# Kernel optimization log

Measured on AMD Instinct MI355X. Metric: run time of the kernel, lower is better.

## Reference

```python
import jax, jax.numpy as jnp
from jax import lax
import numpy as np

DIM = 768
NUM_HEADS = 12
HEAD_DIM = DIM // NUM_HEADS
POOL = 8
LAM1_INIT = 0.5
LAM2_INIT = 0.5
EPS = 1e-6


def rmsnorm(x, w):
    # x / (||x||_2 / sqrt(d) + eps) * w
    d = x.shape[-1]
    rms = jnp.sqrt(jnp.sum(x * x, axis=-1, keepdims=True)) / jnp.sqrt(jnp.asarray(d, x.dtype))
    return x / (rms + EPS) * w


def setup_inputs() -> dict:
    key = jax.random.key(0)
    ks = jax.random.split(key, 10)
    B, H, W = 32, 32, 32
    N = H * W
    x = jax.random.normal(ks[0], (B, N, DIM), dtype=jnp.float32)
    Wqkv = jax.random.normal(ks[1], (3 * DIM, DIM), dtype=jnp.float32) * 0.02
    Wproj = jax.random.normal(ks[2], (DIM, DIM), dtype=jnp.float32) * 0.02
    bproj = jnp.zeros((DIM,), dtype=jnp.float32)
    Wpos = jax.random.normal(ks[3], (HEAD_DIM, HEAD_DIM), dtype=jnp.float32) * 0.02
    Wneg = jax.random.normal(ks[4], (HEAD_DIM, HEAD_DIM), dtype=jnp.float32) * 0.02
    conv_w = jax.random.normal(ks[5], (HEAD_DIM, 1, 3, 3), dtype=jnp.float32) * 0.1  # depthwise OIHW
    lam1 = jnp.asarray(LAM1_INIT, dtype=jnp.float32)
    lam2 = jnp.asarray(LAM2_INIT, dtype=jnp.float32)
    norm1_w = jnp.ones((HEAD_DIM,), dtype=jnp.float32)
    norm2_w = jnp.ones((HEAD_DIM,), dtype=jnp.float32)
    return {"x": x, "Wqkv": Wqkv, "Wproj": Wproj, "bproj": bproj, "Wpos": Wpos,
            "Wneg": Wneg, "conv_w": conv_w, "lam1": lam1, "lam2": lam2,
            "norm1_w": norm1_w, "norm2_w": norm2_w, "H": H, "W": W}


def reference(x, Wqkv, Wproj, bproj, Wpos, Wneg, conv_w, lam1, lam2, norm1_w, norm2_w, H, W):
    B, N, C = x.shape
    h, hd, p = NUM_HEADS, HEAD_DIM, POOL
    scale = hd ** -0.5
    # qkv projection -> [3, B, h, N, hd]
    qkv = (x @ Wqkv.T).reshape(B, N, 3, h, hd).transpose(2, 0, 3, 1, 4)
    q, k, v = qkv[0], qkv[1], qkv[2]
    # depthwise conv + GELU on q in spatial form
    q2 = q.reshape(B, h, H, W, hd).transpose(0, 1, 4, 2, 3).reshape(B * h, hd, H, W)
    qe = lax.conv_general_dilated(q2, conv_w, window_strides=(1, 1), padding='SAME',
                                  feature_group_count=hd,
                                  dimension_numbers=('NCHW', 'OIHW', 'NCHW'))
    qe = jax.nn.gelu(qe, approximate=False)
    # adaptive avg pool to (p, p): exact since H % p == 0
    qp = qe.reshape(B * h, hd, p, H // p, p, W // p).mean(axis=(3, 5))
    t_base = qp.reshape(B, h, hd, p, p).transpose(0, 1, 3, 4, 2).reshape(B, h, p * p, hd)
    # dynamic e+/e- embeddings from global query
    gq = q.mean(axis=2)  # [B, h, hd]
    t_pos = t_base + (gq @ Wpos.T)[:, :, None, :]
    t_neg = t_base + (gq @ Wneg.T)[:, :, None, :]
    # stage 1: pooled contrast tokens attend to k/v
    attn_pos = jax.nn.softmax(jnp.einsum('bhmd,bhnd->bhmn', t_pos, k) * scale, axis=-1)
    v_hat_pos = attn_pos @ v  # [B, h, p*p, hd]
    attn_neg = jax.nn.softmax(jnp.einsum('bhmd,bhnd->bhmn', t_neg, k) * scale, axis=-1)
    v_hat_neg = attn_neg @ v
    v_contrast = rmsnorm(v_hat_pos - lam1 * v_hat_neg, norm1_w) * (1.0 - LAM1_INIT)
    # stage 2: q attends to contrast tokens
    attn1 = jax.nn.softmax(jnp.einsum('bhnd,bhmd->bhnm', q, t_pos) * scale, axis=-1)
    attn2 = jax.nn.softmax(jnp.einsum('bhnd,bhmd->bhnm', q, t_neg) * scale, axis=-1)
    out_patch = (attn1 - lam2 * attn2) @ v_contrast  # [B, h, N, hd]
    out_patch = rmsnorm(out_patch, norm2_w) * (1.0 - LAM2_INIT)
    out_patch = out_patch.transpose(0, 2, 1, 3).reshape(B, N, C)
    out = out_patch @ Wproj.T + bproj
    return out
```

## Files before the change

kernel.cpp:

```cpp
#include <hip/hip_runtime.h>
#include <hip/hip_bf16.h>


typedef __attribute__((ext_vector_type(8))) short short8;
typedef __attribute__((ext_vector_type(4))) short bf16x4;
typedef __attribute__((ext_vector_type(4))) float f32x4;

#define DEV static __device__ __forceinline__

DEV unsigned short f2bf(float f) {
  unsigned int b; __builtin_memcpy(&b, &f, 4);
  unsigned int r = (b + 0x7FFFu + ((b >> 16) & 1u)) >> 16;
  return (unsigned short)r;
}
DEV float bf2f(unsigned short u) {
  unsigned int b = ((unsigned int)u) << 16;
  float f; __builtin_memcpy(&f, &b, 4);
  return f;
}

DEV void gload16(const unsigned short* g, unsigned short* l) {
  __builtin_amdgcn_global_load_lds(
      (const __attribute__((address_space(1))) unsigned int*)g,
      (__attribute__((address_space(3))) unsigned int*)l, 16, 0, 0);
}

DEV void bar() {
  asm volatile("" ::: "memory");
  __builtin_amdgcn_s_barrier();
  asm volatile("" ::: "memory");
}
DEV void wait_vm4() { asm volatile("s_waitcnt vmcnt(4)" ::: "memory"); __builtin_amdgcn_sched_barrier(0); }
DEV void wait_vm0() { asm volatile("s_waitcnt vmcnt(0)" ::: "memory"); __builtin_amdgcn_sched_barrier(0); }
DEV void wait_lgkm0() { asm volatile("s_waitcnt lgkmcnt(0)" ::: "memory"); __builtin_amdgcn_sched_barrier(0); }

constexpr size_t SZ_QKV = (size_t)32 * 12 * 1024 * 64 * 2;
constexpr size_t OFF_Q   = 0;
constexpr size_t OFF_K   = OFF_Q + SZ_QKV;
constexpr size_t OFF_VT  = OFF_K + SZ_QKV;
constexpr size_t OFF_TPB = OFF_VT + SZ_QKV;
constexpr size_t OFF_TNB = OFF_TPB + 3145728;
constexpr size_t OFF_VCT = OFF_TNB + 3145728;
constexpr size_t OFF_OP  = OFF_VCT + 6291456;
constexpr size_t OFF_XB  = OFF_OP + SZ_QKV;
constexpr size_t OFF_WQ  = OFF_XB + SZ_QKV;
constexpr size_t OFF_WP  = OFF_WQ + 3538944;
constexpr size_t OFF_EP  = OFF_WP + 1179648;
constexpr size_t OFF_EN  = OFF_EP + 98304;

__global__ __launch_bounds__(256) void cast_kernel(const float* __restrict__ src,
                                                   unsigned short* __restrict__ dst, int n4) {
  int i = blockIdx.x * 256 + threadIdx.x;
  if (i >= n4) return;
  float4 v = reinterpret_cast<const float4*>(src)[i];
  ushort4 o;
  o.x = f2bf(v.x); o.y = f2bf(v.y); o.z = f2bf(v.z); o.w = f2bf(v.w);
  reinterpret_cast<ushort4*>(dst)[i] = o;
}

DEV void stage_ht(const unsigned short* __restrict__ G, unsigned short* shbase,
                  int grow0, int k0, int htrow0, int w, int lane) {
  const int rl = lane >> 3;
  const int ck = (lane & 7) ^ rl;
  const unsigned short* s0 = G + (size_t)(grow0 + htrow0 + w * 16 + rl) * 768 + k0 + ck * 8;
  gload16(s0, shbase + (htrow0 + w * 16) * 64);
  gload16(s0 + (size_t)8 * 768, shbase + (htrow0 + w * 16 + 8) * 64);
}

__global__ __launch_bounds__(512, 2) void gemm_qkv_kernel(const unsigned short* __restrict__ A,
    const unsigned short* __restrict__ Bm, unsigned short* __restrict__ q,
    unsigned short* __restrict__ k, unsigned short* __restrict__ vt) {
  __shared__ __align__(16) unsigned short sh[65536];
  const int t = threadIdx.x;
  const int lane = t & 63;
  const int w = t >> 6;
  const int wm = w >> 2, wn = w & 3;
  const int l = lane & 15, g = lane >> 4;
  const int id = blockIdx.x;
  const int swz = (id & 7) * 144 + (id >> 3);
  const int rt = swz / 9, ct = swz % 9;
  const int row0 = rt * 256, col0 = ct * 256;

  f32x4 acc[8][4];
#pragma unroll
  for (int i = 0; i < 8; ++i)
#pragma unroll
    for (int j = 0; j < 4; ++j) acc[i][j] = (f32x4){0.f, 0.f, 0.f, 0.f};

  stage_ht(A, sh, row0, 0, 0, w, lane);
  stage_ht(A, sh, row0, 0, 128, w, lane);
  stage_ht(Bm, sh + 32768, col0, 0, 0, w, lane);
  stage_ht(Bm, sh + 32768, col0, 0, 128, w, lane);
  stage_ht(Bm, sh + 32768 + 16384, col0, 64, 0, w, lane);
  stage_ht(Bm, sh + 32768 + 16384, col0, 64, 128, w, lane);
  wait_vm4();
  bar();

  for (int m = 0; m < 12; ++m) {
    const int d = m & 1;
    const unsigned short* Ab = sh + d * 16384;
    const unsigned short* Bb = sh + 32768 + d * 16384;
    short8 af[4][2], bf0[2][2], bf1[2][2];
#pragma unroll
    for (int mt = 0; mt < 4; ++mt)
#pragma unroll
      for (int kc = 0; kc < 2; ++kc) {
        const int r = wm * 128 + mt * 16 + l;
        af[mt][kc] = *reinterpret_cast<const short8*>(Ab + r * 64 + (((kc << 2) | g) ^ (r & 7)) * 8);
      }
#pragma unroll
    for (int nt = 0; nt < 2; ++nt)
#pragma unroll
      for (int kc = 0; kc < 2; ++kc) {
        const int r = wn * 64 + nt * 16 + l;
        bf0[nt][kc] = *reinterpret_cast<const short8*>(Bb + r * 64 + (((kc << 2) | g) ^ (r & 7)) * 8);
      }
    if (m + 1 < 12) stage_ht(A, sh + (d ^ 1) * 16384, row0, (m + 1) * 64, 0, w, lane);
    bar();
    __builtin_amdgcn_s_setprio(1);
#pragma unroll
    for (int kc = 0; kc < 2; ++kc)
#pragma unroll
      for (int mt = 0; mt < 4; ++mt)
#pragma unroll
        for (int nt = 0; nt < 2; ++nt)
          acc[mt][nt] = __builtin_amdgcn_mfma_f32_16x16x32_bf16(af[mt][kc], bf0[nt][kc], acc[mt][nt], 0, 0, 0);
    __builtin_amdgcn_s_setprio(0);
    bar();
#pragma unroll
    for (int nt = 0; nt < 2; ++nt)
#pragma unroll
      for (int kc = 0; kc < 2; ++kc) {
        const int r = wn * 64 + 32 + nt * 16 + l;
        bf1[nt][kc] = *reinterpret_cast<const short8*>(Bb + r * 64 + (((kc << 2) | g) ^ (r & 7)) * 8);
      }
    if (m + 1 < 12) stage_ht(A, sh + (d ^ 1) * 16384, row0, (m + 1) * 64, 128, w, lane);
    bar();
    __builtin_amdgcn_s_setprio(1);
#pragma unroll
    for (int kc = 0; kc < 2; ++kc)
#pragma unroll
      for (int mt = 0; mt < 4; ++mt)
#pragma unroll
        for (int nt = 0; nt < 2; ++nt)
          acc[mt][2 + nt] = __builtin_amdgcn_mfma_f32_16x16x32_bf16(af[mt][kc], bf1[nt][kc], acc[mt][2 + nt], 0, 0, 0);
    __builtin_amdgcn_s_setprio(0);
    bar();
#pragma unroll
    for (int mt = 0; mt < 4; ++mt)
#pragma unroll
      for (int kc = 0; kc < 2; ++kc) {
        const int r = wm * 128 + 64 + mt * 16 + l;
        af[mt][kc] = *reinterpret_cast<const short8*>(Ab + r * 64 + (((kc << 2) | g) ^ (r & 7)) * 8);
      }
    if (m + 2 < 12) stage_ht(Bm, sh + 32768 + d * 16384, col0, (m + 2) * 64, 0, w, lane);
    bar();
    __builtin_amdgcn_s_setprio(1);
#pragma unroll
    for (int kc = 0; kc < 2; ++kc)
#pragma unroll
      for (int mt = 0; mt < 4; ++mt)
#pragma unroll
        for (int nt = 0; nt < 2; ++nt)
          acc[4 + mt][2 + nt] = __builtin_amdgcn_mfma_f32_16x16x32_bf16(af[mt][kc], bf1[nt][kc], acc[4 + mt][2 + nt], 0, 0, 0);
    __builtin_amdgcn_s_setprio(0);
    bar();
    if (m + 2 < 12) stage_ht(Bm, sh + 32768 + d * 16384, col0, (m + 2) * 64, 128, w, lane);
    bar();
    __builtin_amdgcn_s_setprio(1);
#pragma unroll
    for (int kc = 0; kc < 2; ++kc)
#pragma unroll
      for (int mt = 0; mt < 4; ++mt)
#pragma unroll
        for (int nt = 0; nt < 2; ++nt)
          acc[4 + mt][nt] = __builtin_amdgcn_mfma_f32_16x16x32_bf16(af[mt][kc], bf0[nt][kc], acc[4 + mt][nt], 0, 0, 0);
    __builtin_amdgcn_s_setprio(0);
    if (m < 11) {
      if (m == 10) wait_vm0(); else wait_vm4();
    }
    bar();
  }

  const int s_ = ct / 3;
  if (s_ == 2) {
#pragma unroll
    for (int ni = 0; ni < 4; ++ni) {
      const int colg = (ct % 3) * 256 + wn * 64 + ni * 16 + l;
      const int head = colg >> 6, dd = colg & 63;
#pragma unroll
      for (int mi = 0; mi < 8; ++mi) {
        const int row = row0 + wm * 128 + mi * 16 + (g << 2);
        const int b = row >> 10, n = row & 1023;
        ushort4 pk;
        pk.x = f2bf(acc[mi][ni][0]); pk.y = f2bf(acc[mi][ni][1]);
        pk.z = f2bf(acc[mi][ni][2]); pk.w = f2bf(acc[mi][ni][3]);
        *reinterpret_cast<ushort4*>(vt + ((((size_t)b * 12 + head) * 64 + dd) << 10) + n) = pk;
      }
    }
  } else {
    unsigned short* dst = (s_ == 0) ? q : k;
#pragma unroll
    for (int ni = 0; ni < 4; ++ni) {
      const int colg = (ct % 3) * 256 + wn * 64 + ni * 16 + l;
      const int head = colg >> 6, dd = colg & 63;
#pragma unroll
      for (int mi = 0; mi < 8; ++mi) {
#pragma unroll
        for (int r = 0; r < 4; ++r) {
          const int row = row0 + wm * 128 + mi * 16 + (g << 2) + r;
          const int b = row >> 10, n = row & 1023;
          dst[(((size_t)b * 12 + head) * 1024 + n) * 64 + dd] = f2bf(acc[mi][ni][r]);
        }
      }
    }
  }
}

__global__ __launch_bounds__(256) void gq_embed_kernel(const unsigned short* __restrict__ qg,
    const float* __restrict__ Wpos, const float* __restrict__ Wneg,
    float* __restrict__ ep, float* __restrict__ en) {
  const int bh = blockIdx.x;
  const unsigned short* qp = qg + (size_t)bh * 65536;
  __shared__ float red2[32][64];
  __shared__ float gq_s[64];
  const int t = threadIdx.x;
  const int c8 = (t & 7) << 3;
  const int part = t >> 3;
  float s[8] = {0.f, 0.f, 0.f, 0.f, 0.f, 0.f, 0.f, 0.f};
  for (int i = 0; i < 32; ++i) {
    const short8 v = *reinterpret_cast<const short8*>(qp + (size_t)(part * 32 + i) * 64 + c8);
#pragma unroll
    for (int j = 0; j < 8; ++j) s[j] += bf2f((unsigned short)v[j]);
  }
#pragma unroll
  for (int j = 0; j < 8; ++j) red2[part][c8 + j] = s[j];
  __syncthreads();
  if (t < 64) {
    float s2 = 0.f;
    for (int p = 0; p < 32; ++p) s2 += red2[p][t];
    gq_s[t] = s2 * (1.0f / 1024.0f);
  }
  __syncthreads();
  if (t < 128) {
    const int d2 = t & 63;
    const float* Wm = (t < 64) ? Wpos : Wneg;
    float e = 0.f;
    for (int dd = 0; dd < 64; ++dd) e += gq_s[dd] * Wm[d2 * 64 + dd];
    (t < 64 ? ep : en)[bh * 64 + d2] = e;
  }
}

__global__ __launch_bounds__(256) void conv_pool_kernel(const unsigned short* __restrict__ qg,
    const float* __restrict__ conv_w, const float* __restrict__ ep,
    const float* __restrict__ en, unsigned short* __restrict__ t_pos,
    unsigned short* __restrict__ t_neg) {
  const int bh = blockIdx.x;
  const int quad = blockIdx.y;
  const unsigned short* qp = qg + (size_t)bh * 65536;
  __shared__ float pool_s[16][64];
  const int t = threadIdx.x;
  const int dg = t & 7, sp = t >> 3;
  const int d0 = dg << 3;
  float cw[3][3][8];
#pragma unroll
  for (int ky = 0; ky < 3; ++ky)
#pragma unroll
    for (int kx = 0; kx < 3; ++kx)
#pragma unroll
      for (int j = 0; j < 8; ++j)
        cw[ky][kx][j] = conv_w[(d0 + j) * 9 + ky * 3 + kx];
#pragma unroll
  for (int pyl = 0; pyl < 2; ++pyl) {
    float win[8] = {0.f, 0.f, 0.f, 0.f, 0.f, 0.f, 0.f, 0.f};
#pragma unroll
    for (int iy = 0; iy < 4; ++iy) {
      const int y = quad * 8 + pyl * 4 + iy;
      float a[8] = {0.f, 0.f, 0.f, 0.f, 0.f, 0.f, 0.f, 0.f};
#pragma unroll
      for (int ky = 0; ky < 3; ++ky) {
        const int yy = y + ky - 1;
        if (yy < 0 || yy > 31) continue;
#pragma unroll
        for (int kx = 0; kx < 3; ++kx) {
          const int xx = sp + kx - 1;
          if (xx < 0 || xx > 31) continue;
          const short8 v = *reinterpret_cast<const short8*>(qp + (size_t)(yy * 32 + xx) * 64 + d0);
#pragma unroll
          for (int j = 0; j < 8; ++j) a[j] += bf2f((unsigned short)v[j]) * cw[ky][kx][j];
        }
      }
#pragma unroll
      for (int j = 0; j < 8; ++j)
        win[j] += 0.5f * a[j] * (1.0f + erff(a[j] * 0.70710678118654752440f));
    }
#pragma unroll
    for (int j = 0; j < 8; ++j) {
      win[j] += __shfl_xor(win[j], 8);
      win[j] += __shfl_xor(win[j], 16);
    }
    if ((sp & 3) == 0) {
      const int px = sp >> 2;
#pragma unroll
      for (int j = 0; j < 8; ++j) pool_s[pyl * 8 + px][d0 + j] = win[j];
    }
  }
  __syncthreads();
#pragma unroll
  for (int i = 0; i < 4; ++i) {
    const int idx = i * 256 + t;
    const int m = idx >> 6, dd = idx & 63;
    const int mg = quad * 16 + m;
    const float base = pool_s[m][dd] * (1.0f / 16.0f);
    t_pos[(size_t)bh * 4096 + mg * 64 + dd] = f2bf(base + ep[bh * 64 + dd]);
    t_neg[(size_t)bh * 4096 + mg * 64 + dd] = f2bf(base + en[bh * 64 + dd]);
  }
}

__global__ __launch_bounds__(256) void stage1_kernel(const unsigned short* __restrict__ kg,
    const unsigned short* __restrict__ vtg, const unsigned short* __restrict__ tpb,
    const unsigned short* __restrict__ tnb, const float* __restrict__ lam1p,
    const float* __restrict__ norm1_w, unsigned short* __restrict__ vct) {
  const int bh = blockIdx.x;
  __shared__ unsigned short tp[64 * 72], tn[64 * 72];
  __shared__ __align__(16) unsigned short Ks[2][4096];
  __shared__ __align__(16) unsigned short Vts[2][4096];
  const int t = threadIdx.x;
  const int lane = t & 63;
  const int w = t >> 6;
  const int l = lane & 15, g = lane >> 4;
  const size_t kbase = (size_t)bh * 65536;
  const int rl = lane >> 3, ck = (lane & 7) ^ rl;

  for (int L = t; L < 512; L += 256) {
    const int r = L >> 3, c = (L & 7) << 3;
    *reinterpret_cast<short8*>(tp + r * 72 + c) =
        *reinterpret_cast<const short8*>(tpb + (size_t)bh * 4096 + r * 64 + c);
    *reinterpret_cast<short8*>(tn + r * 72 + c) =
        *reinterpret_cast<const short8*>(tnb + (size_t)bh * 4096 + r * 64 + c);
  }
  auto stageKV = [&](int buf, int n0) {
    const unsigned short* ksrc = kg + kbase + (size_t)(n0 + w * 16 + rl) * 64 + ck * 8;
    gload16(ksrc, &Ks[buf][(w * 16) * 64]);
    gload16(ksrc + (size_t)8 * 64, &Ks[buf][(w * 16 + 8) * 64]);
    const unsigned short* vsrc = vtg + kbase + (size_t)(w * 16 + rl) * 1024 + n0 + ck * 8;
    gload16(vsrc, &Vts[buf][(w * 16) * 64]);
    gload16(vsrc + (size_t)8 * 1024, &Vts[buf][(w * 16 + 8) * 64]);
  };
  stageKV(0, 0);
  __syncthreads();

  short8 tf[2][2];
#pragma unroll
  for (int h = 0; h < 2; ++h) {
    tf[0][h] = *reinterpret_cast<const short8*>(tp + (w * 16 + l) * 72 + h * 32 + g * 8);
    tf[1][h] = *reinterpret_cast<const short8*>(tn + (w * 16 + l) * 72 + h * 32 + g * 8);
  }
  float Mo[2] = {-1e30f, -1e30f}, Lo[2] = {0.f, 0.f};
  f32x4 acc[2][4];
#pragma unroll
  for (int pp = 0; pp < 2; ++pp)
#pragma unroll
    for (int dt = 0; dt < 4; ++dt) acc[pp][dt] = (f32x4){0.f, 0.f, 0.f, 0.f};

  for (int it = 0; it < 16; ++it) {
    const int buf = it & 1;
    if (it < 15) stageKV(buf ^ 1, (it + 1) * 64);
    short8 kf[4][2];
#pragma unroll
    for (int tile = 0; tile < 4; ++tile)
#pragma unroll
      for (int h = 0; h < 2; ++h) {
        const int R = tile * 16 + l;
        kf[tile][h] = *reinterpret_cast<const short8*>(&Ks[buf][R * 64 + ((((h << 2) | g)) ^ (l & 7)) * 8]);
      }
    bf16x4 pf[2][4];
#pragma unroll
    for (int pp = 0; pp < 2; ++pp) {
      f32x4 s[4];
#pragma unroll
      for (int tile = 0; tile < 4; ++tile) {
        s[tile] = (f32x4){0.f, 0.f, 0.f, 0.f};
#pragma unroll
        for (int h = 0; h < 2; ++h)
          s[tile] = __builtin_amdgcn_mfma_f32_16x16x32_bf16(kf[tile][h], tf[pp][h], s[tile], 0, 0, 0);
      }
      float p[4][4];
      float tmax = -1e30f;
#pragma unroll
      for (int tile = 0; tile < 4; ++tile)
#pragma unroll
        for (int r = 0; r < 4; ++r) {
          const float v = s[tile][r] * 0.125f;
          p[tile][r] = v;
          tmax = fmaxf(tmax, v);
        }
      tmax = fmaxf(tmax, __shfl_xor(tmax, 16));
      tmax = fmaxf(tmax, __shfl_xor(tmax, 32));
      const float nm = fmaxf(Mo[pp], tmax);
      const float al = __expf(Mo[pp] - nm);
      Mo[pp] = nm;
      float ps = 0.f;
#pragma unroll
      for (int tile = 0; tile < 4; ++tile)
#pragma unroll
        for (int r = 0; r < 4; ++r) {
          const float e = __expf(p[tile][r] - nm);
          p[tile][r] = e;
          ps += e;
        }
      ps += __shfl_xor(ps, 16);
      ps += __shfl_xor(ps, 32);
      Lo[pp] = Lo[pp] * al + ps;
#pragma unroll
      for (int tile = 0; tile < 4; ++tile) {
        bf16x4 pk;
        pk[0] = (short)f2bf(p[tile][0]); pk[1] = (short)f2bf(p[tile][1]);
        pk[2] = (short)f2bf(p[tile][2]); pk[3] = (short)f2bf(p[tile][3]);
        pf[pp][tile] = pk;
      }
      float ar[4];
#pragma unroll
      for (int r = 0; r < 4; ++r) ar[r] = __shfl(al, 4 * g + r);
#pragma unroll
      for (int dt = 0; dt < 4; ++dt)
#pragma unroll
        for (int r = 0; r < 4; ++r) acc[pp][dt][r] *= ar[r];
    }
#pragma unroll
    for (int tile = 0; tile < 4; ++tile)
#pragma unroll
      for (int dt = 0; dt < 4; ++dt) {
        const int R = dt * 16 + l;
        const bf16x4 vf = *reinterpret_cast<const bf16x4*>(
            &Vts[buf][R * 64 + (((2 * tile + (g >> 1)) ^ (l & 7)) * 8) + (g & 1) * 4]);
        acc[0][dt] = __builtin_amdgcn_mfma_f32_16x16x16bf16_1k(pf[0][tile], vf, acc[0][dt], 0, 0, 0);
        acc[1][dt] = __builtin_amdgcn_mfma_f32_16x16x16bf16_1k(pf[1][tile], vf, acc[1][dt], 0, 0, 0);
      }
    __syncthreads();
  }
  const float inv0 = 1.f / Lo[0], inv1 = 1.f / Lo[1];
  float i1r[4], i2r[4];
#pragma unroll
  for (int r = 0; r < 4; ++r) {
    i1r[r] = __shfl(inv0, 4 * g + r);
    i2r[r] = __shfl(inv1, 4 * g + r);
  }
  const float lam1 = lam1p[0];
  float od[4][4], ss[4] = {0.f, 0.f, 0.f, 0.f};
#pragma unroll
  for (int dt = 0; dt < 4; ++dt)
#pragma unroll
    for (int r = 0; r < 4; ++r) {
      const float v = acc[0][dt][r] * i1r[r] - lam1 * (acc[1][dt][r] * i2r[r]);
      od[dt][r] = v;
      ss[r] += v * v;
    }
#pragma unroll
  for (int r = 0; r < 4; ++r) {
    ss[r] += __shfl_xor(ss[r], 1);
    ss[r] += __shfl_xor(ss[r], 2);
    ss[r] += __shfl_xor(ss[r], 4);
    ss[r] += __shfl_xor(ss[r], 8);
  }
  float sc[4];
#pragma unroll
  for (int r = 0; r < 4; ++r) sc[r] = 0.5f / (sqrtf(ss[r]) * 0.125f + 1e-6f);
  const int mb = w * 16 + 4 * g;
#pragma unroll
  for (int dt = 0; dt < 4; ++dt) {
    const int dd = dt * 16 + l;
    const float nw = norm1_w[dd];
    ushort4 pk;
    pk.x = f2bf(od[dt][0] * sc[0] * nw);
    pk.y = f2bf(od[dt][1] * sc[1] * nw);
    pk.z = f2bf(od[dt][2] * sc[2] * nw);
    pk.w = f2bf(od[dt][3] * sc[3] * nw);
    *reinterpret_cast<ushort4*>(vct + (size_t)bh * 4096 + dd * 64 + mb) = pk;
  }
}

__global__ __launch_bounds__(256) void stage2_kernel(const unsigned short* __restrict__ qg,
    const unsigned short* __restrict__ tpb, const unsigned short* __restrict__ tnb,
    const unsigned short* __restrict__ vctg, const float* __restrict__ lam2p,
    const float* __restrict__ norm2_w, unsigned short* __restrict__ opb) {
  const int bh = blockIdx.x;
  const int q0 = blockIdx.y * 64;
  __shared__ unsigned short tp[64 * 72], tn[64 * 72], Qs[64 * 72], Vc[64 * 72];
  const int t = threadIdx.x;
  const int lane = t & 63;
  const int w = t >> 6;
  const int l = lane & 15, g = lane >> 4;
  for (int L = t; L < 512; L += 256) {
    const int r = L >> 3, c = (L & 7) << 3;
    *reinterpret_cast<short8*>(tp + r * 72 + c) =
        *reinterpret_cast<const short8*>(tpb + (size_t)bh * 4096 + r * 64 + c);
    *reinterpret_cast<short8*>(tn + r * 72 + c) =
        *reinterpret_cast<const short8*>(tnb + (size_t)bh * 4096 + r * 64 + c);
    *reinterpret_cast<short8*>(Qs + r * 72 + c) =
        *reinterpret_cast<const short8*>(qg + (size_t)bh * 65536 + (size_t)(q0 + r) * 64 + c);
    *reinterpret_cast<short8*>(Vc + r * 72 + c) =
        *reinterpret_cast<const short8*>(vctg + (size_t)bh * 4096 + r * 64 + c);
  }
  __syncthreads();
  short8 qf[2];
#pragma unroll
  for (int h = 0; h < 2; ++h)
    qf[h] = *reinterpret_cast<const short8*>(Qs + (w * 16 + l) * 72 + h * 32 + g * 8);
  bf16x4 vcf[4][4];
#pragma unroll
  for (int tile = 0; tile < 4; ++tile)
#pragma unroll
    for (int dt = 0; dt < 4; ++dt)
      vcf[tile][dt] = *reinterpret_cast<const bf16x4*>(Vc + (dt * 16 + l) * 72 + tile * 16 + g * 4);
  bf16x4 pf[2][4];
#pragma unroll
  for (int pp = 0; pp < 2; ++pp) {
    const unsigned short* tm = pp ? tn : tp;
    f32x4 s[4];
#pragma unroll
    for (int tile = 0; tile < 4; ++tile) {
      s[tile] = (f32x4){0.f, 0.f, 0.f, 0.f};
#pragma unroll
      for (int h = 0; h < 2; ++h) {
        const short8 tfb = *reinterpret_cast<const short8*>(tm + (tile * 16 + l) * 72 + h * 32 + g * 8);
        s[tile] = __builtin_amdgcn_mfma_f32_16x16x32_bf16(tfb, qf[h], s[tile], 0, 0, 0);
      }
    }
    float p[4][4];
    float lmax = -1e30f;
#pragma unroll
    for (int tile = 0; tile < 4; ++tile)
#pragma unroll
      for (int r = 0; r < 4; ++r) {
        const float v = s[tile][r] * 0.125f;
        p[tile][r] = v;
        lmax = fmaxf(lmax, v);
      }
    lmax = fmaxf(lmax, __shfl_xor(lmax, 16));
    lmax = fmaxf(lmax, __shfl_xor(lmax, 32));
    float ps = 0.f;
#pragma unroll
    for (int tile = 0; tile < 4; ++tile)
#pragma unroll
      for (int r = 0; r < 4; ++r) {
        const float e = __expf(p[tile][r] - lmax);
        p[tile][r] = e;
        ps += e;
      }
    ps += __shfl_xor(ps, 16);
    ps += __shfl_xor(ps, 32);
    const float inv = 1.f / ps;
#pragma unroll
    for (int tile = 0; tile < 4; ++tile) {
      bf16x4 pk;
      pk[0] = (short)f2bf(p[tile][0] * inv); pk[1] = (short)f2bf(p[tile][1] * inv);
      pk[2] = (short)f2bf(p[tile][2] * inv); pk[3] = (short)f2bf(p[tile][3] * inv);
      pf[pp][tile] = pk;
    }
  }
  f32x4 a1[4], a2[4];
#pragma unroll
  for (int dt = 0; dt < 4; ++dt) {
    a1[dt] = (f32x4){0.f, 0.f, 0.f, 0.f};
    a2[dt] = (f32x4){0.f, 0.f, 0.f, 0.f};
  }
#pragma unroll
  for (int tile = 0; tile < 4; ++tile)
#pragma unroll
    for (int dt = 0; dt < 4; ++dt) {
      a1[dt] = __builtin_amdgcn_mfma_f32_16x16x16bf16_1k(pf[0][tile], vcf[tile][dt], a1[dt], 0, 0, 0);
      a2[dt] = __builtin_amdgcn_mfma_f32_16x16x16bf16_1k(pf[1][tile], vcf[tile][dt], a2[dt], 0, 0, 0);
    }
  const float lam2 = lam2p[0];
  float od[4][4], ss[4] = {0.f, 0.f, 0.f, 0.f};
#pragma unroll
  for (int dt = 0; dt < 4; ++dt)
#pragma unroll
    for (int r = 0; r < 4; ++r) {
      const float v = a1[dt][r] - lam2 * a2[dt][r];
      od[dt][r] = v;
      ss[r] += v * v;
    }
#pragma unroll
  for (int r = 0; r < 4; ++r) {
    ss[r] += __shfl_xor(ss[r], 1);
    ss[r] += __shfl_xor(ss[r], 2);
    ss[r] += __shfl_xor(ss[r], 4);
    ss[r] += __shfl_xor(ss[r], 8);
  }
  float sc[4];
#pragma unroll
  for (int r = 0; r < 4; ++r) sc[r] = 0.5f / (sqrtf(ss[r]) * 0.125f + 1e-6f);
  const int b = bh / 12, head = bh % 12;
  const size_t ob = ((size_t)b * 1024 + q0 + w * 16 + 4 * g) * 768 + head * 64;
#pragma unroll
  for (int dt = 0; dt < 4; ++dt) {
    const float nw = norm2_w[dt * 16 + l];
#pragma unroll
    for (int r = 0; r < 4; ++r)
      opb[ob + (size_t)r * 768 + dt * 16 + l] = f2bf(od[dt][r] * sc[r] * nw);
  }
}

__global__ __launch_bounds__(512, 2) void gemm_proj_kernel(const unsigned short* __restrict__ A,
    const unsigned short* __restrict__ Bm, const float* __restrict__ bias,
    float* __restrict__ out) {
  __shared__ __align__(16) unsigned short sh[49152];
  const int t = threadIdx.x;
  const int lane = t & 63;
  const int w = t >> 6;
  const int wm = w >> 2, wn = w & 3;
  const int l = lane & 15, g = lane >> 4;
  const int id = blockIdx.x;
  const int swz = (id & 7) * 96 + (id >> 3);
  const int rt = swz / 3, ct = swz % 3;
  const int row0 = rt * 128, col0 = ct * 256;

  f32x4 acc[4][4];
#pragma unroll
  for (int i = 0; i < 4; ++i)
#pragma unroll
    for (int j = 0; j < 4; ++j) acc[i][j] = (f32x4){0.f, 0.f, 0.f, 0.f};

  stage_ht(A, sh, row0, 0, 0, w, lane);
  stage_ht(Bm, sh + 16384, col0, 0, 0, w, lane);
  stage_ht(Bm, sh + 16384, col0, 0, 128, w, lane);
  stage_ht(Bm, sh + 32768, col0, 64, 0, w, lane);
  stage_ht(Bm, sh + 32768, col0, 64, 128, w, lane);
  wait_vm4();
  bar();

  for (int m = 0; m < 12; ++m) {
    const int d = m & 1;
    const unsigned short* Ab = sh + d * 8192;
    const unsigned short* Bb = sh + 16384 + d * 16384;
    short8 af[4][2], bfv[4][2];
#pragma unroll
    for (int mt = 0; mt < 4; ++mt)
#pragma unroll
      for (int kc = 0; kc < 2; ++kc) {
        const int r = wm * 64 + mt * 16 + l;
        af[mt][kc] = *reinterpret_cast<const short8*>(Ab + r * 64 + (((kc << 2) | g) ^ (r & 7)) * 8);
      }
#pragma unroll
    for (int nt = 0; nt < 2; ++nt)
#pragma unroll
      for (int kc = 0; kc < 2; ++kc) {
        const int r = wn * 64 + nt * 16 + l;
        bfv[nt][kc] = *reinterpret_cast<const short8*>(Bb + r * 64 + (((kc << 2) | g) ^ (r & 7)) * 8);
      }
    if (m + 1 < 12) stage_ht(A, sh + (d ^ 1) * 8192, row0, (m + 1) * 64, 0, w, lane);
    bar();
    __builtin_amdgcn_s_setprio(1);
#pragma unroll
    for (int kc = 0; kc < 2; ++kc)
#pragma unroll
      for (int mt = 0; mt < 4; ++mt)
#pragma unroll
        for (int nt = 0; nt < 2; ++nt)
          acc[mt][nt] = __builtin_amdgcn_mfma_f32_16x16x32_bf16(af[mt][kc], bfv[nt][kc], acc[mt][nt], 0, 0, 0);
    __builtin_amdgcn_s_setprio(0);
    bar();
#pragma unroll
    for (int nt = 2; nt < 4; ++nt)
#pragma unroll
      for (int kc = 0; kc < 2; ++kc) {
        const int r = wn * 64 + nt * 16 + l;
        bfv[nt][kc] = *reinterpret_cast<const short8*>(Bb + r * 64 + (((kc << 2) | g) ^ (r & 7)) * 8);
      }
    wait_lgkm0();
    bar();
    if (m + 2 < 12) {
      stage_ht(Bm, sh + 16384 + d * 16384, col0, (m + 2) * 64, 0, w, lane);
      stage_ht(Bm, sh + 16384 + d * 16384, col0, (m + 2) * 64, 128, w, lane);
    }
    __builtin_amdgcn_s_setprio(1);
#pragma unroll
    for (int kc = 0; kc < 2; ++kc)
#pragma unroll
      for (int mt = 0; mt < 4; ++mt)
#pragma unroll
        for (int nt = 2; nt < 4; ++nt)
          acc[mt][nt] = __builtin_amdgcn_mfma_f32_16x16x32_bf16(af[mt][kc], bfv[nt][kc], acc[mt][nt], 0, 0, 0);
    __builtin_amdgcn_s_setprio(0);
    if (m < 11) {
      if (m == 10) wait_vm0(); else wait_vm4();
    }
    bar();
  }
#pragma unroll
  for (int ni = 0; ni < 4; ++ni) {
    const int colg = ct * 256 + wn * 64 + ni * 16 + l;
    const float bv = bias[colg];
#pragma unroll
    for (int mi = 0; mi < 4; ++mi)
#pragma unroll
      for (int r = 0; r < 4; ++r) {
        const int row = row0 + wm * 64 + mi * 16 + (g << 2) + r;
        out[(size_t)row * 768 + colg] = acc[mi][ni][r] + bv;
      }
  }
}

extern "C" void kernel_launch(void* const* d_in, const int* in_sizes, int n_in,
                              void* d_out, int out_size, void* d_ws, size_t ws_size,
                              hipStream_t stream) {
  (void)in_sizes; (void)n_in; (void)out_size; (void)ws_size;
  const float* x       = (const float*)d_in[0];
  const float* Wqkv    = (const float*)d_in[1];
  const float* Wproj   = (const float*)d_in[2];
  const float* bproj   = (const float*)d_in[3];
  const float* Wpos    = (const float*)d_in[4];
  const float* Wneg    = (const float*)d_in[5];
  const float* conv_w  = (const float*)d_in[6];
  const float* lam1    = (const float*)d_in[7];
  const float* lam2    = (const float*)d_in[8];
  const float* norm1_w = (const float*)d_in[9];
  const float* norm2_w = (const float*)d_in[10];
  float* out = (float*)d_out;
  char* ws = (char*)d_ws;
  unsigned short* qb   = (unsigned short*)(ws + OFF_Q);
  unsigned short* kb   = (unsigned short*)(ws + OFF_K);
  unsigned short* vtb  = (unsigned short*)(ws + OFF_VT);
  unsigned short* tpbb = (unsigned short*)(ws + OFF_TPB);
  unsigned short* tnbb = (unsigned short*)(ws + OFF_TNB);
  unsigned short* vctb = (unsigned short*)(ws + OFF_VCT);
  unsigned short* opb  = (unsigned short*)(ws + OFF_OP);
  unsigned short* xb   = (unsigned short*)(ws + OFF_XB);
  unsigned short* wqb  = (unsigned short*)(ws + OFF_WQ);
  unsigned short* wpb  = (unsigned short*)(ws + OFF_WP);
  float* epb           = (float*)(ws + OFF_EP);
  float* enb           = (float*)(ws + OFF_EN);

  cast_kernel<<<dim3(6291456 / 256), dim3(256), 0, stream>>>(x, xb, 6291456);
  cast_kernel<<<dim3(442368 / 256), dim3(256), 0, stream>>>(Wqkv, wqb, 442368);
  cast_kernel<<<dim3(147456 / 256), dim3(256), 0, stream>>>(Wproj, wpb, 147456);
  gemm_qkv_kernel<<<dim3(1152), dim3(512), 0, stream>>>(xb, wqb, qb, kb, vtb);
  gq_embed_kernel<<<dim3(384), dim3(256), 0, stream>>>(qb, Wpos, Wneg, epb, enb);
  conv_pool_kernel<<<dim3(384, 4), dim3(256), 0, stream>>>(qb, conv_w, epb, enb, tpbb, tnbb);
  stage1_kernel<<<dim3(384), dim3(256), 0, stream>>>(kb, vtb, tpbb, tnbb, lam1, norm1_w, vctb);
  stage2_kernel<<<dim3(384, 16), dim3(256), 0, stream>>>(qb, tpbb, tnbb, vctb, lam2, norm2_w, opb);
  gemm_proj_kernel<<<dim3(768), dim3(512), 0, stream>>>(opb, wpb, bproj, out);
}
```

Before: 389.4 us.

## Merge cast launches, load stage1 tokens directly, and give stage2 blocks more rows

The three fp32-to-bf16 cast kernels become one launch that picks its source and destination by global index. Stage1 now loads its pooled-token fragments straight from global memory into registers, dropping the shared-memory staging buffers. Stage2 blocks now handle 256 query rows in four sub-iterations instead of 64, so the t_pos, t_neg and v_contrast tiles and the norm weights are loaded once per 256 rows. The trade-off is four times fewer stage2 blocks and a larger shared-memory footprint per block, which may reduce occupancy.

Result: no change. 391.5 us (+0.5%).

```diff
diff --git a/kernel.cpp b/kernel.cpp
--- a/kernel.cpp
+++ b/kernel.cpp
@@ -48,14 +48,19 @@
 constexpr size_t OFF_EP  = OFF_WP + 1179648;
 constexpr size_t OFF_EN  = OFF_EP + 98304;
 
-__global__ __launch_bounds__(256) void cast_kernel(const float* __restrict__ src,
-                                                   unsigned short* __restrict__ dst, int n4) {
-  int i = blockIdx.x * 256 + threadIdx.x;
-  if (i >= n4) return;
-  float4 v = reinterpret_cast<const float4*>(src)[i];
+__global__ __launch_bounds__(256) void cast3_kernel(const float* __restrict__ x,
+    const float* __restrict__ wq, const float* __restrict__ wp,
+    unsigned short* __restrict__ xd, unsigned short* __restrict__ wqd,
+    unsigned short* __restrict__ wpd) {
+  const int i = blockIdx.x * 256 + threadIdx.x;
+  const float* src; unsigned short* dst; int off;
+  if (i < 6291456) { src = x; dst = xd; off = i; }
+  else if (i < 6733824) { src = wq; dst = wqd; off = i - 6291456; }
+  else { src = wp; dst = wpd; off = i - 6733824; }
+  float4 v = reinterpret_cast<const float4*>(src)[off];
   ushort4 o;
   o.x = f2bf(v.x); o.y = f2bf(v.y); o.z = f2bf(v.z); o.w = f2bf(v.w);
-  reinterpret_cast<ushort4*>(dst)[i] = o;
+  reinterpret_cast<ushort4*>(dst)[off] = o;
 }
 
 DEV void stage_ht(const unsigned short* __restrict__ G, unsigned short* shbase,
@@ -322,7 +327,6 @@
     const unsigned short* __restrict__ tnb, const float* __restrict__ lam1p,
     const float* __restrict__ norm1_w, unsigned short* __restrict__ vct) {
   const int bh = blockIdx.x;
-  __shared__ unsigned short tp[64 * 72], tn[64 * 72];
   __shared__ __align__(16) unsigned short Ks[2][4096];
   __shared__ __align__(16) unsigned short Vts[2][4096];
   const int t = threadIdx.x;
@@ -332,12 +336,11 @@
   const size_t kbase = (size_t)bh * 65536;
   const int rl = lane >> 3, ck = (lane & 7) ^ rl;
 
-  for (int L = t; L < 512; L += 256) {
-    const int r = L >> 3, c = (L & 7) << 3;
-    *reinterpret_cast<short8*>(tp + r * 72 + c) =
-        *reinterpret_cast<const short8*>(tpb + (size_t)bh * 4096 + r * 64 + c);
-    *reinterpret_cast<short8*>(tn + r * 72 + c) =
-        *reinterpret_cast<const short8*>(tnb + (size_t)bh * 4096 + r * 64 + c);
+  short8 tf[2][2];
+#pragma unroll
+  for (int h = 0; h < 2; ++h) {
+    tf[0][h] = *reinterpret_cast<const short8*>(tpb + (size_t)bh * 4096 + (w * 16 + l) * 64 + h * 32 + g * 8);
+    tf[1][h] = *reinterpret_cast<const short8*>(tnb + (size_t)bh * 4096 + (w * 16 + l) * 64 + h * 32 + g * 8);
   }
   auto stageKV = [&](int buf, int n0) {
     const unsigned short* ksrc = kg + kbase + (size_t)(n0 + w * 16 + rl) * 64 + ck * 8;
@@ -350,12 +353,6 @@
   stageKV(0, 0);
   __syncthreads();
 
-  short8 tf[2][2];
-#pragma unroll
-  for (int h = 0; h < 2; ++h) {
-    tf[0][h] = *reinterpret_cast<const short8*>(tp + (w * 16 + l) * 72 + h * 32 + g * 8);
-    tf[1][h] = *reinterpret_cast<const short8*>(tn + (w * 16 + l) * 72 + h * 32 + g * 8);
-  }
   float Mo[2] = {-1e30f, -1e30f}, Lo[2] = {0.f, 0.f};
   f32x4 acc[2][4];
 #pragma unroll
@@ -485,8 +482,9 @@
     const unsigned short* __restrict__ vctg, const float* __restrict__ lam2p,
     const float* __restrict__ norm2_w, unsigned short* __restrict__ opb) {
   const int bh = blockIdx.x;
-  const int q0 = blockIdx.y * 64;
-  __shared__ unsigned short tp[64 * 72], tn[64 * 72], Qs[64 * 72], Vc[64 * 72];
+  const int q0 = blockIdx.y * 256;
+  __shared__ unsigned short tp[64 * 72], tn[64 * 72], Vc[64 * 72];
+  __shared__ unsigned short Qs[256 * 72];
   const int t = threadIdx.x;
   const int lane = t & 63;
   const int w = t >> 6;
@@ -497,109 +495,118 @@
         *reinterpret_cast<const short8*>(tpb + (size_t)bh * 4096 + r * 64 + c);
     *reinterpret_cast<short8*>(tn + r * 72 + c) =
         *reinterpret_cast<const short8*>(tnb + (size_t)bh * 4096 + r * 64 + c);
+    *reinterpret_cast<short8*>(Vc + r * 72 + c) =
+        *reinterpret_cast<const short8*>(vctg + (size_t)bh * 4096 + r * 64 + c);
+  }
+  for (int L = t; L < 2048; L += 256) {
+    const int r = L >> 3, c = (L & 7) << 3;
     *reinterpret_cast<short8*>(Qs + r * 72 + c) =
         *reinterpret_cast<const short8*>(qg + (size_t)bh * 65536 + (size_t)(q0 + r) * 64 + c);
-    *reinterpret_cast<short8*>(Vc + r * 72 + c) =
-        *reinterpret_cast<const short8*>(vctg + (size_t)bh * 4096 + r * 64 + c);
   }
   __syncthreads();
-  short8 qf[2];
-#pragma unroll
-  for (int h = 0; h < 2; ++h)
-    qf[h] = *reinterpret_cast<const short8*>(Qs + (w * 16 + l) * 72 + h * 32 + g * 8);
   bf16x4 vcf[4][4];
 #pragma unroll
   for (int tile = 0; tile < 4; ++tile)
 #pragma unroll
     for (int dt = 0; dt < 4; ++dt)
       vcf[tile][dt] = *reinterpret_cast<const bf16x4*>(Vc + (dt * 16 + l) * 72 + tile * 16 + g * 4);
-  bf16x4 pf[2][4];
-#pragma unroll
-  for (int pp = 0; pp < 2; ++pp) {
-    const unsigned short* tm = pp ? tn : tp;
-    f32x4 s[4];
-#pragma unroll
-    for (int tile = 0; tile < 4; ++tile) {
-      s[tile] = (f32x4){0.f, 0.f, 0.f, 0.f};
-#pragma unroll
-      for (int h = 0; h < 2; ++h) {
-        const short8 tfb = *reinterpret_cast<const short8*>(tm + (tile * 16 + l) * 72 + h * 32 + g * 8);
-        s[tile] = __builtin_amdgcn_mfma_f32_16x16x32_bf16(tfb, qf[h], s[tile], 0, 0, 0);
-      }
-    }
-    float p[4][4];
-    float lmax = -1e30f;
+  const float lam2 = lam2p[0];
+  const int b = bh / 12, head = bh % 12;
+  float nw[4];
+#pragma unroll
+  for (int dt = 0; dt < 4; ++dt) nw[dt] = norm2_w[dt * 16 + l];
+
+  for (int s = 0; s < 4; ++s) {
+    const int rrow = (w * 4 + s) * 16;
+    short8 qf[2];
+#pragma unroll
+    for (int h = 0; h < 2; ++h)
+      qf[h] = *reinterpret_cast<const short8*>(Qs + (rrow + l) * 72 + h * 32 + g * 8);
+    bf16x4 pf[2][4];
+#pragma unroll
+    for (int pp = 0; pp < 2; ++pp) {
+      const unsigned short* tm = pp ? tn : tp;
+      f32x4 sv[4];
+#pragma unroll
+      for (int tile = 0; tile < 4; ++tile) {
+        sv[tile] = (f32x4){0.f, 0.f, 0.f, 0.f};
+#pragma unroll
+        for (int h = 0; h < 2; ++h) {
+          const short8 tfb = *reinterpret_cast<const short8*>(tm + (tile * 16 + l) * 72 + h * 32 + g * 8);
+          sv[tile] = __builtin_amdgcn_mfma_f32_16x16x32_bf16(tfb, qf[h], sv[tile], 0, 0, 0);
+        }
+      }
+      float p[4][4];
+      float lmax = -1e30f;
+#pragma unroll
+      for (int tile = 0; tile < 4; ++tile)
+#pragma unroll
+        for (int r = 0; r < 4; ++r) {
+          const float v = sv[tile][r] * 0.125f;
+          p[tile][r] = v;
+          lmax = fmaxf(lmax, v);
+        }
+      lmax = fmaxf(lmax, __shfl_xor(lmax, 16));
+      lmax = fmaxf(lmax, __shfl_xor(lmax, 32));
+      float ps = 0.f;
+#pragma unroll
+      for (int tile = 0; tile < 4; ++tile)
+#pragma unroll
+        for (int r = 0; r < 4; ++r) {
+          const float e = __expf(p[tile][r] - lmax);
+          p[tile][r] = e;
+          ps += e;
+        }
+      ps += __shfl_xor(ps, 16);
+      ps += __shfl_xor(ps, 32);
+      const float inv = 1.f / ps;
+#pragma unroll
+      for (int tile = 0; tile < 4; ++tile) {
+        bf16x4 pk;
+        pk[0] = (short)f2bf(p[tile][0] * inv); pk[1] = (short)f2bf(p[tile][1] * inv);
+        pk[2] = (short)f2bf(p[tile][2] * inv); pk[3] = (short)f2bf(p[tile][3] * inv);
+        pf[pp][tile] = pk;
+      }
+    }
+    f32x4 a1[4], a2[4];
+#pragma unroll
+    for (int dt = 0; dt < 4; ++dt) {
+      a1[dt] = (f32x4){0.f, 0.f, 0.f, 0.f};
+      a2[dt] = (f32x4){0.f, 0.f, 0.f, 0.f};
+    }
 #pragma unroll
     for (int tile = 0; tile < 4; ++tile)
 #pragma unroll
+      for (int dt = 0; dt < 4; ++dt) {
+        a1[dt] = __builtin_amdgcn_mfma_f32_16x16x16bf16_1k(pf[0][tile], vcf[tile][dt], a1[dt], 0, 0, 0);
+        a2[dt] = __builtin_amdgcn_mfma_f32_16x16x16bf16_1k(pf[1][tile], vcf[tile][dt], a2[dt], 0, 0, 0);
+      }
+    float od[4][4], ss[4] = {0.f, 0.f, 0.f, 0.f};
+#pragma unroll
+    for (int dt = 0; dt < 4; ++dt)
+#pragma unroll
       for (int r = 0; r < 4; ++r) {
-        const float v = s[tile][r] * 0.125f;
-        p[tile][r] = v;
-        lmax = fmaxf(lmax, v);
-      }
-    lmax = fmaxf(lmax, __shfl_xor(lmax, 16));
-    lmax = fmaxf(lmax, __shfl_xor(lmax, 32));
-    float ps = 0.f;
-#pragma unroll
-    for (int tile = 0; tile < 4; ++tile)
-#pragma unroll
-      for (int r = 0; r < 4; ++r) {
-        const float e = __expf(p[tile][r] - lmax);
-        p[tile][r] = e;
-        ps += e;
-      }
-    ps += __shfl_xor(ps, 16);
-    ps += __shfl_xor(ps, 32);
-    const float inv = 1.f / ps;
-#pragma unroll
-    for (int tile = 0; tile < 4; ++tile) {
-      bf16x4 pk;
-      pk[0] = (short)f2bf(p[tile][0] * inv); pk[1] = (short)f2bf(p[tile][1] * inv);
-      pk[2] = (short)f2bf(p[tile][2] * inv); pk[3] = (short)f2bf(p[tile][3] * inv);
-      pf[pp][tile] = pk;
-    }
-  }
-  f32x4 a1[4], a2[4];
-#pragma unroll
-  for (int dt = 0; dt < 4; ++dt) {
-    a1[dt] = (f32x4){0.f, 0.f, 0.f, 0.f};
-    a2[dt] = (f32x4){0.f, 0.f, 0.f, 0.f};
-  }
-#pragma unroll
-  for (int tile = 0; tile < 4; ++tile)
+        const float v = a1[dt][r] - lam2 * a2[dt][r];
+        od[dt][r] = v;
+        ss[r] += v * v;
+      }
+#pragma unroll
+    for (int r = 0; r < 4; ++r) {
+      ss[r] += __shfl_xor(ss[r], 1);
+      ss[r] += __shfl_xor(ss[r], 2);
+      ss[r] += __shfl_xor(ss[r], 4);
+      ss[r] += __shfl_xor(ss[r], 8);
+    }
+    float sc[4];
+#pragma unroll
+    for (int r = 0; r < 4; ++r) sc[r] = 0.5f / (sqrtf(ss[r]) * 0.125f + 1e-6f);
+    const size_t ob = ((size_t)b * 1024 + q0 + rrow + 4 * g) * 768 + head * 64;
 #pragma unroll
     for (int dt = 0; dt < 4; ++dt) {
-      a1[dt] = __builtin_amdgcn_mfma_f32_16x16x16bf16_1k(pf[0][tile], vcf[tile][dt], a1[dt], 0, 0, 0);
-      a2[dt] = __builtin_amdgcn_mfma_f32_16x16x16bf16_1k(pf[1][tile], vcf[tile][dt], a2[dt], 0, 0, 0);
-    }
-  const float lam2 = lam2p[0];
-  float od[4][4], ss[4] = {0.f, 0.f, 0.f, 0.f};
-#pragma unroll
-  for (int dt = 0; dt < 4; ++dt)
-#pragma unroll
-    for (int r = 0; r < 4; ++r) {
-      const float v = a1[dt][r] - lam2 * a2[dt][r];
-      od[dt][r] = v;
-      ss[r] += v * v;
-    }
-#pragma unroll
-  for (int r = 0; r < 4; ++r) {
-    ss[r] += __shfl_xor(ss[r], 1);
-    ss[r] += __shfl_xor(ss[r], 2);
-    ss[r] += __shfl_xor(ss[r], 4);
-    ss[r] += __shfl_xor(ss[r], 8);
-  }
-  float sc[4];
-#pragma unroll
-  for (int r = 0; r < 4; ++r) sc[r] = 0.5f / (sqrtf(ss[r]) * 0.125f + 1e-6f);
-  const int b = bh / 12, head = bh % 12;
-  const size_t ob = ((size_t)b * 1024 + q0 + w * 16 + 4 * g) * 768 + head * 64;
-#pragma unroll
-  for (int dt = 0; dt < 4; ++dt) {
-    const float nw = norm2_w[dt * 16 + l];
-#pragma unroll
-    for (int r = 0; r < 4; ++r)
-      opb[ob + (size_t)r * 768 + dt * 16 + l] = f2bf(od[dt][r] * sc[r] * nw);
+#pragma unroll
+      for (int r = 0; r < 4; ++r)
+        opb[ob + (size_t)r * 768 + dt * 16 + l] = f2bf(od[dt][r] * sc[r] * nw[dt]);
+    }
   }
 }
 
@@ -733,13 +740,11 @@
   float* epb           = (float*)(ws + OFF_EP);
   float* enb           = (float*)(ws + OFF_EN);
 
-  cast_kernel<<<dim3(6291456 / 256), dim3(256), 0, stream>>>(x, xb, 6291456);
-  cast_kernel<<<dim3(442368 / 256), dim3(256), 0, stream>>>(Wqkv, wqb, 442368);
-  cast_kernel<<<dim3(147456 / 256), dim3(256), 0, stream>>>(Wproj, wpb, 147456);
+  cast3_kernel<<<dim3(26880), dim3(256), 0, stream>>>(x, Wqkv, Wproj, xb, wqb, wpb);
   gemm_qkv_kernel<<<dim3(1152), dim3(512), 0, stream>>>(xb, wqb, qb, kb, vtb);
   gq_embed_kernel<<<dim3(384), dim3(256), 0, stream>>>(qb, Wpos, Wneg, epb, enb);
   conv_pool_kernel<<<dim3(384, 4), dim3(256), 0, stream>>>(qb, conv_w, epb, enb, tpbb, tnbb);
   stage1_kernel<<<dim3(384), dim3(256), 0, stream>>>(kb, vtb, tpbb, tnbb, lam1, norm1_w, vctb);
-  stage2_kernel<<<dim3(384, 16), dim3(256), 0, stream>>>(qb, tpbb, tnbb, vctb, lam2, norm2_w, opb);
+  stage2_kernel<<<dim3(384, 4), dim3(256), 0, stream>>>(qb, tpbb, tnbb, vctb, lam2, norm2_w, opb);
   gemm_proj_kernel<<<dim3(768), dim3(512), 0, stream>>>(opb, wpb, bproj, out);
 }
```
